# Optimization experiments

Measured on AMD Instinct MI355X. Metric: run time of the kernel, lower is better.

## Reference

```python
import jax, jax.numpy as jnp
import numpy as np

D_MODEL = 1024
D_K = 64
D_V = 64
TEMPERATURE = float(np.sqrt(D_K))
LN_EPS = 1e-5


def setup_inputs() -> dict:
    key = jax.random.key(0)
    ks = jax.random.split(key, 8)
    B, L = 8, 2048
    q = jax.random.normal(ks[0], (B, L, D_K), dtype=jnp.float32)
    k = jax.random.normal(ks[1], (B, L, D_K), dtype=jnp.float32)
    v = jax.random.normal(ks[2], (B, L, D_V), dtype=jnp.float32)
    residual = jax.random.normal(ks[3], (B, L, D_MODEL), dtype=jnp.float32)
    # fc: Linear(d_v, d_model), xavier-normal weight, zero-ish bias
    fc_w = jax.random.normal(ks[4], (D_MODEL, D_V), dtype=jnp.float32) * float(np.sqrt(2.0 / (D_V + D_MODEL)))
    fc_b = jnp.zeros((D_MODEL,), dtype=jnp.float32)
    ln_gamma = jnp.ones((D_MODEL,), dtype=jnp.float32)
    ln_beta = jnp.zeros((D_MODEL,), dtype=jnp.float32)
    return {"q": q, "k": k, "v": v, "residual": residual,
            "fc_w": fc_w, "fc_b": fc_b, "ln_gamma": ln_gamma, "ln_beta": ln_beta}


def reference(q, k, v, residual, fc_w, fc_b, ln_gamma, ln_beta):
    # scaled dot-product attention: scores [B, Lq, Lk]
    scores = jnp.einsum("bqd,bkd->bqk", q, k) / TEMPERATURE
    # module computes both log_softmax and softmax (shared logsumexp in a
    # fused kernel); log_attn is discarded by Attention.forward
    log_attn = jax.nn.log_softmax(scores, axis=2)
    attn = jnp.exp(log_attn)  # == softmax(scores); dropout is identity at eval
    out = jnp.einsum("bqk,bkv->bqv", attn, v)  # [B, Lq, d_v]
    # fc + residual + LayerNorm (dropout identity at eval)
    out = jnp.einsum("bqv,mv->bqm", out, fc_w) + fc_b
    x = out + residual
    mu = jnp.mean(x, axis=-1, keepdims=True)
    var = jnp.var(x, axis=-1, keepdims=True)
    return (x - mu) * jax.lax.rsqrt(var + LN_EPS) * ln_gamma + ln_beta
```

## Files before the change

### kernel.cpp

```cpp
#include <hip/hip_runtime.h>

typedef float  f32x4 __attribute__((ext_vector_type(4)));
typedef float  f4v   __attribute__((ext_vector_type(4)));
typedef short  s16x8 __attribute__((ext_vector_type(8)));
typedef unsigned short u16x4 __attribute__((ext_vector_type(4)));
typedef unsigned short u16x8 __attribute__((ext_vector_type(8)));
typedef unsigned short u16;

#define DEVI static __device__ __forceinline__
#define AS1 __attribute__((address_space(1)))
#define AS3 __attribute__((address_space(3)))

DEVI u16 f2bf(float f) {
  unsigned int u = __builtin_bit_cast(unsigned int, f);
  u += 0x7FFFu + ((u >> 16) & 1u);
  return (u16)(u >> 16);
}

constexpr int B  = 8;
constexpr int L  = 2048;
constexpr int D  = 64;
constexpr int DM = 1024;

__global__ void prep_kernel(const float* __restrict__ k, const float* __restrict__ v,
                            const float* __restrict__ w,
                            u16* __restrict__ kbf, u16* __restrict__ vtbf,
                            u16* __restrict__ wbf) {
  __shared__ float tile[64 * 65];
  const int bid = blockIdx.x, tid = threadIdx.x;
  if (bid < 1024) {
    const int i = bid * 256 + tid;
    f4v f = ((const f4v*)k)[i];
    u16x4 o;
#pragma unroll
    for (int j = 0; j < 4; ++j) o[j] = f2bf(f[j] * 0.18033688f);
    ((u16x4*)kbf)[i] = o;
  } else if (bid < 1024 + 64) {
    const int i = (bid - 1024) * 256 + tid;
    f4v f = ((const f4v*)w)[i];
    u16x4 o;
#pragma unroll
    for (int j = 0; j < 4; ++j) o[j] = f2bf(f[j]);
    ((u16x4*)wbf)[i] = o;
  } else {
    const int t2 = bid - 1088;
    const int b = t2 >> 5, tt = t2 & 31;
    const float* vp = v + ((size_t)b * L + tt * 64) * D;
    for (int i = tid; i < 4096; i += 256) {
      const int r = i >> 6, c = i & 63;
      tile[c * 65 + r] = vp[i];
    }
    __syncthreads();
    u16* op = vtbf + (size_t)b * D * L + tt * 64;
    for (int i = tid; i < 4096; i += 256) {
      const int dv = i >> 6, kv = i & 63;
      op[(size_t)dv * L + kv] = f2bf(tile[dv * 65 + kv]);
    }
  }
}

__global__ __launch_bounds__(512) void attn_kernel(const float* __restrict__ q,
                                                   const u16* __restrict__ kbf,
                                                   const u16* __restrict__ vtbf,
                                                   u16* __restrict__ Og) {
  __shared__ __align__(16) char smem[58 * 1024];
  u16*   Kt   = (u16*)smem;
  u16*   Vt   = (u16*)(smem + 24 * 1024);
  u16*   Pl   = (u16*)(smem + 48 * 1024);
  float* Macc = (float*)smem;
  float* Lsum = (float*)(smem + 35 * 1024);

  const int blk = blockIdx.x;
  const int b = blk & 7;
  const int qrow0 = (blk >> 3) * 64;
  const int tid = threadIdx.x;
  const int wave = tid >> 6, lane = tid & 63;
  const int g = wave >> 1, h = wave & 1;
  const int lg = lane >> 4, ln = lane & 15;

  s16x8 aq[2];
  {
    const float* qp = q + ((size_t)b * L + qrow0 + g * 16 + ln) * D + lg * 8;
#pragma unroll
    for (int kk = 0; kk < 2; ++kk) {
      f4v f0 = *(const f4v*)(qp + kk * 32);
      f4v f1 = *(const f4v*)(qp + kk * 32 + 4);
      s16x8 a;
#pragma unroll
      for (int j = 0; j < 4; ++j) { a[j] = (short)f2bf(f0[j]); a[4 + j] = (short)f2bf(f1[j]); }
      aq[kk] = a;
    }
  }

  const f32x4 zf = {0.f, 0.f, 0.f, 0.f};
  f32x4 acc[4];
#pragma unroll
  for (int i = 0; i < 4; ++i) acc[i] = zf;
  float lrow[4] = {0.f, 0.f, 0.f, 0.f};

  const u16* kb = kbf + (size_t)b * L * D;
  const u16* vb = vtbf + (size_t)b * D * L;

  auto stage = [&](int t) {
    const int buf = t % 3;
    const int kv0 = t * 64;
    const int row = tid >> 3, jl = tid & 7;
    const int js = jl ^ (row & 7);
    const u16* srcK = kb + (size_t)(kv0 + row) * D + js * 8;
    __builtin_amdgcn_global_load_lds(
        (const AS1 unsigned int*)srcK, (AS3 unsigned int*)&Kt[buf * 4096 + tid * 8], 16, 0, 0);
    const u16* srcV = vb + (size_t)row * L + kv0 + js * 8;
    __builtin_amdgcn_global_load_lds(
        (const AS1 unsigned int*)srcV, (AS3 unsigned int*)&Vt[buf * 4096 + tid * 8], 16, 0, 0);
  };

  stage(0);
  stage(1);

  for (int t = 0; t < 32; ++t) {
    if (t < 31) { asm volatile("s_waitcnt vmcnt(2)" ::: "memory"); }
    else        { asm volatile("s_waitcnt vmcnt(0)" ::: "memory"); }
    __builtin_amdgcn_sched_barrier(0);
    __builtin_amdgcn_s_barrier();
    __builtin_amdgcn_sched_barrier(0);
    if (t + 2 < 32) stage(t + 2);
    const int buf = t % 3;

    f32x4 s[2];
    s[0] = zf; s[1] = zf;
#pragma unroll
    for (int kk = 0; kk < 2; ++kk) {
#pragma unroll
      for (int fn2 = 0; fn2 < 2; ++fn2) {
        const int kvr = h * 32 + fn2 * 16 + ln;
        const int j = (kk * 4 + lg) ^ (kvr & 7);
        s16x8 bk = *(const s16x8*)&Kt[buf * 4096 + kvr * 64 + j * 8];
        s[fn2] = __builtin_amdgcn_mfma_f32_16x16x32_bf16(aq[kk], bk, s[fn2], 0, 0, 0);
      }
    }

#pragma unroll
    for (int r = 0; r < 4; ++r) {
      const float p0 = __builtin_amdgcn_exp2f(s[0][r]);
      const float p1 = __builtin_amdgcn_exp2f(s[1][r]);
      lrow[r] += p0 + p1;
      Pl[wave * 640 + (lg * 4 + r) * 40 + ln]      = f2bf(p0);
      Pl[wave * 640 + (lg * 4 + r) * 40 + 16 + ln] = f2bf(p1);
    }

    asm volatile("" ::: "memory");

    s16x8 ap = *(const s16x8*)&Pl[wave * 640 + ln * 40 + lg * 8];
#pragma unroll
    for (int fn = 0; fn < 4; ++fn) {
      const int dv = fn * 16 + ln;
      const int j = (h * 4 + lg) ^ (dv & 7);
      s16x8 bv = *(const s16x8*)&Vt[buf * 4096 + dv * 64 + j * 8];
      acc[fn] = __builtin_amdgcn_mfma_f32_16x16x32_bf16(ap, bv, acc[fn], 0, 0, 0);
    }
  }

  __syncthreads();

#pragma unroll
  for (int r = 0; r < 4; ++r) {
#pragma unroll
    for (int off = 1; off < 16; off <<= 1) lrow[r] += __shfl_xor(lrow[r], off, 64);
    if (ln == 0) Lsum[wave * 16 + lg * 4 + r] = lrow[r];
  }
#pragma unroll
  for (int fn = 0; fn < 4; ++fn)
#pragma unroll
    for (int r = 0; r < 4; ++r)
      Macc[wave * 1088 + (lg * 4 + r) * 68 + fn * 16 + ln] = acc[fn][r];
  __syncthreads();

  {
    const int row = tid >> 3, d0 = (tid & 7) * 8;
    const int g2 = row >> 4, r2 = row & 15;
    const float linv = 1.f / (Lsum[(g2 * 2) * 16 + r2] + Lsum[(g2 * 2 + 1) * 16 + r2]);
    const float* m0p = &Macc[(g2 * 2) * 1088 + r2 * 68 + d0];
    const float* m1p = &Macc[(g2 * 2 + 1) * 1088 + r2 * 68 + d0];
    f4v o0 = *(const f4v*)(m0p)     + *(const f4v*)(m1p);
    f4v o1 = *(const f4v*)(m0p + 4) + *(const f4v*)(m1p + 4);
    u16x8 ob;
#pragma unroll
    for (int j = 0; j < 4; ++j) {
      ob[j]     = f2bf(o0[j] * linv);
      ob[4 + j] = f2bf(o1[j] * linv);
    }
    *(u16x8*)(Og + ((size_t)b * L + qrow0 + row) * D + d0) = ob;
  }
}

__global__ __launch_bounds__(512, 2) void fc_ln_kernel(const u16* __restrict__ Og,
                                                       const u16* __restrict__ wbf,
                                                       const float* __restrict__ bias,
                                                       const float* __restrict__ resid,
                                                       const float* __restrict__ gamma,
                                                       const float* __restrict__ beta,
                                                       float* __restrict__ out) {
  __shared__ __align__(16) u16   Wl[1024 * 64];
  __shared__ __align__(16) float bl[1024];
  __shared__ __align__(16) float gl[1024];
  __shared__ __align__(16) float btl[1024];
  __shared__ float part[8][16][2];

  const int tid = threadIdx.x;
  const int wave = tid >> 6, lane = tid & 63;
  const int rg = wave >> 2, mq = wave & 3;
  const int lg = lane >> 4, ln = lane & 15;
  const int m0 = mq * 256;
  const int vblk = (blockIdx.x & 7) * 32 + (blockIdx.x >> 3);
  const int rowA = vblk * 64 + rg * 16 + ln;
  const int rowB = rowA + 32;
  const int jb = ln & 7;

  {
#pragma unroll
    for (int i = 0; i < 16; ++i) {
      const int c = tid + i * 512;
      const int r = c >> 3, j = c & 7;
      const u16* src = wbf + r * 64 + (j ^ (r & 7)) * 8;
      __builtin_amdgcn_global_load_lds(
          (const AS1 unsigned int*)src, (AS3 unsigned int*)&Wl[c * 8], 16, 0, 0);
    }
    if (tid < 256) {
      __builtin_amdgcn_global_load_lds(
          (const AS1 unsigned int*)(bias + tid * 4), (AS3 unsigned int*)&bl[tid * 4], 16, 0, 0);
      __builtin_amdgcn_global_load_lds(
          (const AS1 unsigned int*)(beta + tid * 4), (AS3 unsigned int*)&btl[tid * 4], 16, 0, 0);
    } else {
      const int t2 = tid - 256;
      __builtin_amdgcn_global_load_lds(
          (const AS1 unsigned int*)(gamma + t2 * 4), (AS3 unsigned int*)&gl[t2 * 4], 16, 0, 0);
    }
  }

  f4v boAr0, boAr1;
  {
    const u16* opA = Og + (size_t)rowA * D + lg * 8;
    asm volatile("global_load_dwordx4 %0, %1, off"           : "=v"(boAr0) : "v"(opA) : "memory");
    asm volatile("global_load_dwordx4 %0, %1, off offset:64" : "=v"(boAr1) : "v"(opA) : "memory");
  }
  f4v rsdA[16];
  {
    const float* rp = resid + (size_t)rowA * DM + m0 + lg * 4;
#pragma unroll
    for (int fn = 0; fn < 16; ++fn)
      asm volatile("global_load_dwordx4 %0, %1, off offset:%c2"
                   : "=v"(rsdA[fn]) : "v"(rp), "i"(fn * 64) : "memory");
  }

  asm volatile("s_waitcnt vmcnt(0)" ::: "memory");
  __builtin_amdgcn_sched_barrier(0);
  __builtin_amdgcn_s_barrier();
  __builtin_amdgcn_sched_barrier(0);

  f32x4 acc[16];
#pragma unroll
  for (int fn = 0; fn < 16; ++fn)
    acc[fn] = *(const f4v*)&bl[m0 + fn * 16 + lg * 4] + rsdA[fn];

  f4v boBr0, boBr1;
  {
    const u16* opB = Og + (size_t)rowB * D + lg * 8;
    asm volatile("global_load_dwordx4 %0, %1, off"           : "=v"(boBr0) : "v"(opB) : "memory");
    asm volatile("global_load_dwordx4 %0, %1, off offset:64" : "=v"(boBr1) : "v"(opB) : "memory");
  }
  f4v rsdB[16];
  {
    const float* rp = resid + (size_t)rowB * DM + m0 + lg * 4;
#pragma unroll
    for (int fn = 0; fn < 16; ++fn)
      asm volatile("global_load_dwordx4 %0, %1, off offset:%c2"
                   : "=v"(rsdB[fn]) : "v"(rp), "i"(fn * 64) : "memory");
  }

  {
    const s16x8 bo0 = __builtin_bit_cast(s16x8, boAr0);
    const s16x8 bo1 = __builtin_bit_cast(s16x8, boAr1);
#pragma unroll
    for (int fn = 0; fn < 16; ++fn) {
      const int m = m0 + fn * 16 + ln;
      s16x8 aw0 = *(const s16x8*)&Wl[m * 64 + (lg ^ jb) * 8];
      s16x8 aw1 = *(const s16x8*)&Wl[m * 64 + ((4 + lg) ^ jb) * 8];
      acc[fn] = __builtin_amdgcn_mfma_f32_16x16x32_bf16(aw0, bo0, acc[fn], 0, 0, 0);
      acc[fn] = __builtin_amdgcn_mfma_f32_16x16x32_bf16(aw1, bo1, acc[fn], 0, 0, 0);
    }
    float sum = 0.f, ssq = 0.f;
#pragma unroll
    for (int fn = 0; fn < 16; ++fn)
#pragma unroll
      for (int r = 0; r < 4; ++r) { const float x = acc[fn][r]; sum += x; ssq += x * x; }
    sum += __shfl_xor(sum, 16, 64); ssq += __shfl_xor(ssq, 16, 64);
    sum += __shfl_xor(sum, 32, 64); ssq += __shfl_xor(ssq, 32, 64);
    if (lg == 0) { part[wave][ln][0] = sum; part[wave][ln][1] = ssq; }
    asm volatile("s_waitcnt lgkmcnt(0)" ::: "memory");
    __builtin_amdgcn_s_barrier();
    __builtin_amdgcn_sched_barrier(0);
    float sm = 0.f, q2 = 0.f;
#pragma unroll
    for (int w2 = 0; w2 < 4; ++w2) { sm += part[rg * 4 + w2][ln][0]; q2 += part[rg * 4 + w2][ln][1]; }
    const float mu   = sm * (1.0f / 1024.0f);
    const float var  = q2 * (1.0f / 1024.0f) - mu * mu;
    const float rstd = rsqrtf(var + 1e-5f);
#pragma unroll
    for (int fn = 0; fn < 16; ++fn) {
      const int m4 = m0 + fn * 16 + lg * 4;
      const f4v gm = *(const f4v*)&gl[m4];
      const f4v bt = *(const f4v*)&btl[m4];
      f4v o;
#pragma unroll
      for (int r = 0; r < 4; ++r) o[r] = (acc[fn][r] - mu) * rstd * gm[r] + bt[r];
      *(f4v*)&out[(size_t)rowA * DM + m4] = o;
    }
  }

  asm volatile("s_waitcnt vmcnt(0)" ::: "memory");
  __builtin_amdgcn_sched_barrier(0);
  __builtin_amdgcn_s_barrier();
  __builtin_amdgcn_sched_barrier(0);

  {
#pragma unroll
    for (int fn = 0; fn < 16; ++fn)
      acc[fn] = *(const f4v*)&bl[m0 + fn * 16 + lg * 4] + rsdB[fn];
    const s16x8 bo0 = __builtin_bit_cast(s16x8, boBr0);
    const s16x8 bo1 = __builtin_bit_cast(s16x8, boBr1);
#pragma unroll
    for (int fn = 0; fn < 16; ++fn) {
      const int m = m0 + fn * 16 + ln;
      s16x8 aw0 = *(const s16x8*)&Wl[m * 64 + (lg ^ jb) * 8];
      s16x8 aw1 = *(const s16x8*)&Wl[m * 64 + ((4 + lg) ^ jb) * 8];
      acc[fn] = __builtin_amdgcn_mfma_f32_16x16x32_bf16(aw0, bo0, acc[fn], 0, 0, 0);
      acc[fn] = __builtin_amdgcn_mfma_f32_16x16x32_bf16(aw1, bo1, acc[fn], 0, 0, 0);
    }
    float sum = 0.f, ssq = 0.f;
#pragma unroll
    for (int fn = 0; fn < 16; ++fn)
#pragma unroll
      for (int r = 0; r < 4; ++r) { const float x = acc[fn][r]; sum += x; ssq += x * x; }
    sum += __shfl_xor(sum, 16, 64); ssq += __shfl_xor(ssq, 16, 64);
    sum += __shfl_xor(sum, 32, 64); ssq += __shfl_xor(ssq, 32, 64);
    if (lg == 0) { part[wave][ln][0] = sum; part[wave][ln][1] = ssq; }
    asm volatile("s_waitcnt lgkmcnt(0)" ::: "memory");
    __builtin_amdgcn_s_barrier();
    __builtin_amdgcn_sched_barrier(0);
    float sm = 0.f, q2 = 0.f;
#pragma unroll
    for (int w2 = 0; w2 < 4; ++w2) { sm += part[rg * 4 + w2][ln][0]; q2 += part[rg * 4 + w2][ln][1]; }
    const float mu   = sm * (1.0f / 1024.0f);
    const float var  = q2 * (1.0f / 1024.0f) - mu * mu;
    const float rstd = rsqrtf(var + 1e-5f);
#pragma unroll
    for (int fn = 0; fn < 16; ++fn) {
      const int m4 = m0 + fn * 16 + lg * 4;
      const f4v gm = *(const f4v*)&gl[m4];
      const f4v bt = *(const f4v*)&btl[m4];
      f4v o;
#pragma unroll
      for (int r = 0; r < 4; ++r) o[r] = (acc[fn][r] - mu) * rstd * gm[r] + bt[r];
      *(f4v*)&out[(size_t)rowB * DM + m4] = o;
    }
  }
}

extern "C" void kernel_launch(void* const* d_in, const int* in_sizes, int n_in,
                              void* d_out, int out_size, void* d_ws, size_t ws_size,
                              hipStream_t stream) {
  const float* q     = (const float*)d_in[0];
  const float* k     = (const float*)d_in[1];
  const float* v     = (const float*)d_in[2];
  const float* resid = (const float*)d_in[3];
  const float* fc_w  = (const float*)d_in[4];
  const float* fc_b  = (const float*)d_in[5];
  const float* gamma = (const float*)d_in[6];
  const float* beta  = (const float*)d_in[7];
  float* out = (float*)d_out;

  char* ws = (char*)d_ws;
  u16*   kbf  = (u16*)(ws);
  u16*   vtbf = (u16*)(ws + (2u << 20));
  u16*   wbf  = (u16*)(ws + (4u << 20));
  u16*   Og   = (u16*)(ws + (4u << 20) + (128u << 10));

  prep_kernel<<<1344, 256, 0, stream>>>(k, v, fc_w, kbf, vtbf, wbf);
  attn_kernel<<<256, 512, 0, stream>>>(q, kbf, vtbf, Og);
  fc_ln_kernel<<<256, 512, 0, stream>>>(Og, wbf, fc_b, resid, gamma, beta, out);
}
```

Before: 58.28 us.

## Drop LDS weight staging in fc_ln; use small 16-row blocks reading weights from cache

```diff
diff --git a/kernel.cpp b/kernel.cpp
--- a/kernel.cpp
+++ b/kernel.cpp
@@ -193,63 +193,47 @@
   }
 }
 
-__global__ __launch_bounds__(512, 2) void fc_ln_kernel(const u16* __restrict__ Og,
+__global__ __launch_bounds__(256, 3) void fc_ln_kernel(const u16* __restrict__ Og,
                                                        const u16* __restrict__ wbf,
                                                        const float* __restrict__ bias,
                                                        const float* __restrict__ resid,
                                                        const float* __restrict__ gamma,
                                                        const float* __restrict__ beta,
                                                        float* __restrict__ out) {
-  __shared__ __align__(16) u16   Wl[1024 * 64];
   __shared__ __align__(16) float bl[1024];
   __shared__ __align__(16) float gl[1024];
   __shared__ __align__(16) float btl[1024];
-  __shared__ float part[8][16][2];
+  __shared__ float part[4][16][2];
 
   const int tid = threadIdx.x;
   const int wave = tid >> 6, lane = tid & 63;
-  const int rg = wave >> 2, mq = wave & 3;
   const int lg = lane >> 4, ln = lane & 15;
-  const int m0 = mq * 256;
-  const int vblk = (blockIdx.x & 7) * 32 + (blockIdx.x >> 3);
-  const int rowA = vblk * 64 + rg * 16 + ln;
-  const int rowB = rowA + 32;
+  const int m0 = wave * 256;
+  const int vblk = (blockIdx.x & 7) * 128 + (blockIdx.x >> 3);
+  const int row = vblk * 16 + ln;
   const int jb = ln & 7;
-
+  (void)jb;
+
+  __builtin_amdgcn_global_load_lds(
+      (const AS1 unsigned int*)(bias + tid * 4), (AS3 unsigned int*)&bl[tid * 4], 16, 0, 0);
+  __builtin_amdgcn_global_load_lds(
+      (const AS1 unsigned int*)(gamma + tid * 4), (AS3 unsigned int*)&gl[tid * 4], 16, 0, 0);
+  __builtin_amdgcn_global_load_lds(
+      (const AS1 unsigned int*)(beta + tid * 4), (AS3 unsigned int*)&btl[tid * 4], 16, 0, 0);
+
+  f4v bo0r, bo1r;
   {
-#pragma unroll
-    for (int i = 0; i < 16; ++i) {
-      const int c = tid + i * 512;
-      const int r = c >> 3, j = c & 7;
-      const u16* src = wbf + r * 64 + (j ^ (r & 7)) * 8;
-      __builtin_amdgcn_global_load_lds(
-          (const AS1 unsigned int*)src, (AS3 unsigned int*)&Wl[c * 8], 16, 0, 0);
-    }
-    if (tid < 256) {
-      __builtin_amdgcn_global_load_lds(
-          (const AS1 unsigned int*)(bias + tid * 4), (AS3 unsigned int*)&bl[tid * 4], 16, 0, 0);
-      __builtin_amdgcn_global_load_lds(
-          (const AS1 unsigned int*)(beta + tid * 4), (AS3 unsigned int*)&btl[tid * 4], 16, 0, 0);
-    } else {
-      const int t2 = tid - 256;
-      __builtin_amdgcn_global_load_lds(
-          (const AS1 unsigned int*)(gamma + t2 * 4), (AS3 unsigned int*)&gl[t2 * 4], 16, 0, 0);
-    }
-  }
-
-  f4v boAr0, boAr1;
+    const u16* op = Og + (size_t)row * D + lg * 8;
+    asm volatile("global_load_dwordx4 %0, %1, off"           : "=v"(bo0r) : "v"(op) : "memory");
+    asm volatile("global_load_dwordx4 %0, %1, off offset:64" : "=v"(bo1r) : "v"(op) : "memory");
+  }
+  f4v rsd[16];
   {
-    const u16* opA = Og + (size_t)rowA * D + lg * 8;
-    asm volatile("global_load_dwordx4 %0, %1, off"           : "=v"(boAr0) : "v"(opA) : "memory");
-    asm volatile("global_load_dwordx4 %0, %1, off offset:64" : "=v"(boAr1) : "v"(opA) : "memory");
-  }
-  f4v rsdA[16];
-  {
-    const float* rp = resid + (size_t)rowA * DM + m0 + lg * 4;
+    const float* rp = resid + (size_t)row * DM + m0 + lg * 4;
 #pragma unroll
     for (int fn = 0; fn < 16; ++fn)
       asm volatile("global_load_dwordx4 %0, %1, off offset:%c2"
-                   : "=v"(rsdA[fn]) : "v"(rp), "i"(fn * 64) : "memory");
+                   : "=v"(rsd[fn]) : "v"(rp), "i"(fn * 64) : "memory");
   }
 
   asm volatile("s_waitcnt vmcnt(0)" ::: "memory");
@@ -257,112 +241,45 @@
   __builtin_amdgcn_s_barrier();
   __builtin_amdgcn_sched_barrier(0);
 
+  const s16x8 bo0 = __builtin_bit_cast(s16x8, bo0r);
+  const s16x8 bo1 = __builtin_bit_cast(s16x8, bo1r);
   f32x4 acc[16];
 #pragma unroll
+  for (int fn = 0; fn < 16; ++fn) {
+    const int m = m0 + fn * 16;
+    const u16* wp = &wbf[(size_t)(m + ln) * D + lg * 8];
+    s16x8 aw0 = *(const s16x8*)(wp);
+    s16x8 aw1 = *(const s16x8*)(wp + 32);
+    acc[fn] = *(const f4v*)&bl[m + lg * 4] + rsd[fn];
+    acc[fn] = __builtin_amdgcn_mfma_f32_16x16x32_bf16(aw0, bo0, acc[fn], 0, 0, 0);
+    acc[fn] = __builtin_amdgcn_mfma_f32_16x16x32_bf16(aw1, bo1, acc[fn], 0, 0, 0);
+  }
+
+  float sum = 0.f, ssq = 0.f;
+#pragma unroll
   for (int fn = 0; fn < 16; ++fn)
-    acc[fn] = *(const f4v*)&bl[m0 + fn * 16 + lg * 4] + rsdA[fn];
-
-  f4v boBr0, boBr1;
-  {
-    const u16* opB = Og + (size_t)rowB * D + lg * 8;
-    asm volatile("global_load_dwordx4 %0, %1, off"           : "=v"(boBr0) : "v"(opB) : "memory");
-    asm volatile("global_load_dwordx4 %0, %1, off offset:64" : "=v"(boBr1) : "v"(opB) : "memory");
-  }
-  f4v rsdB[16];
-  {
-    const float* rp = resid + (size_t)rowB * DM + m0 + lg * 4;
-#pragma unroll
-    for (int fn = 0; fn < 16; ++fn)
-      asm volatile("global_load_dwordx4 %0, %1, off offset:%c2"
-                   : "=v"(rsdB[fn]) : "v"(rp), "i"(fn * 64) : "memory");
-  }
-
-  {
-    const s16x8 bo0 = __builtin_bit_cast(s16x8, boAr0);
-    const s16x8 bo1 = __builtin_bit_cast(s16x8, boAr1);
-#pragma unroll
-    for (int fn = 0; fn < 16; ++fn) {
-      const int m = m0 + fn * 16 + ln;
-      s16x8 aw0 = *(const s16x8*)&Wl[m * 64 + (lg ^ jb) * 8];
-      s16x8 aw1 = *(const s16x8*)&Wl[m * 64 + ((4 + lg) ^ jb) * 8];
-      acc[fn] = __builtin_amdgcn_mfma_f32_16x16x32_bf16(aw0, bo0, acc[fn], 0, 0, 0);
-      acc[fn] = __builtin_amdgcn_mfma_f32_16x16x32_bf16(aw1, bo1, acc[fn], 0, 0, 0);
-    }
-    float sum = 0.f, ssq = 0.f;
-#pragma unroll
-    for (int fn = 0; fn < 16; ++fn)
-#pragma unroll
-      for (int r = 0; r < 4; ++r) { const float x = acc[fn][r]; sum += x; ssq += x * x; }
-    sum += __shfl_xor(sum, 16, 64); ssq += __shfl_xor(ssq, 16, 64);
-    sum += __shfl_xor(sum, 32, 64); ssq += __shfl_xor(ssq, 32, 64);
-    if (lg == 0) { part[wave][ln][0] = sum; part[wave][ln][1] = ssq; }
-    asm volatile("s_waitcnt lgkmcnt(0)" ::: "memory");
-    __builtin_amdgcn_s_barrier();
-    __builtin_amdgcn_sched_barrier(0);
-    float sm = 0.f, q2 = 0.f;
-#pragma unroll
-    for (int w2 = 0; w2 < 4; ++w2) { sm += part[rg * 4 + w2][ln][0]; q2 += part[rg * 4 + w2][ln][1]; }
-    const float mu   = sm * (1.0f / 1024.0f);
-    const float var  = q2 * (1.0f / 1024.0f) - mu * mu;
-    const float rstd = rsqrtf(var + 1e-5f);
-#pragma unroll
-    for (int fn = 0; fn < 16; ++fn) {
-      const int m4 = m0 + fn * 16 + lg * 4;
-      const f4v gm = *(const f4v*)&gl[m4];
-      const f4v bt = *(const f4v*)&btl[m4];
-      f4v o;
-#pragma unroll
-      for (int r = 0; r < 4; ++r) o[r] = (acc[fn][r] - mu) * rstd * gm[r] + bt[r];
-      *(f4v*)&out[(size_t)rowA * DM + m4] = o;
-    }
-  }
-
-  asm volatile("s_waitcnt vmcnt(0)" ::: "memory");
-  __builtin_amdgcn_sched_barrier(0);
-  __builtin_amdgcn_s_barrier();
-  __builtin_amdgcn_sched_barrier(0);
-
-  {
-#pragma unroll
-    for (int fn = 0; fn < 16; ++fn)
-      acc[fn] = *(const f4v*)&bl[m0 + fn * 16 + lg * 4] + rsdB[fn];
-    const s16x8 bo0 = __builtin_bit_cast(s16x8, boBr0);
-    const s16x8 bo1 = __builtin_bit_cast(s16x8, boBr1);
-#pragma unroll
-    for (int fn = 0; fn < 16; ++fn) {
-      const int m = m0 + fn * 16 + ln;
-      s16x8 aw0 = *(const s16x8*)&Wl[m * 64 + (lg ^ jb) * 8];
-      s16x8 aw1 = *(const s16x8*)&Wl[m * 64 + ((4 + lg) ^ jb) * 8];
-      acc[fn] = __builtin_amdgcn_mfma_f32_16x16x32_bf16(aw0, bo0, acc[fn], 0, 0, 0);
-      acc[fn] = __builtin_amdgcn_mfma_f32_16x16x32_bf16(aw1, bo1, acc[fn], 0, 0, 0);
-    }
-    float sum = 0.f, ssq = 0.f;
-#pragma unroll
-    for (int fn = 0; fn < 16; ++fn)
-#pragma unroll
-      for (int r = 0; r < 4; ++r) { const float x = acc[fn][r]; sum += x; ssq += x * x; }
-    sum += __shfl_xor(sum, 16, 64); ssq += __shfl_xor(ssq, 16, 64);
-    sum += __shfl_xor(sum, 32, 64); ssq += __shfl_xor(ssq, 32, 64);
-    if (lg == 0) { part[wave][ln][0] = sum; part[wave][ln][1] = ssq; }
-    asm volatile("s_waitcnt lgkmcnt(0)" ::: "memory");
-    __builtin_amdgcn_s_barrier();
-    __builtin_amdgcn_sched_barrier(0);
-    float sm = 0.f, q2 = 0.f;
-#pragma unroll
-    for (int w2 = 0; w2 < 4; ++w2) { sm += part[rg * 4 + w2][ln][0]; q2 += part[rg * 4 + w2][ln][1]; }
-    const float mu   = sm * (1.0f / 1024.0f);
-    const float var  = q2 * (1.0f / 1024.0f) - mu * mu;
-    const float rstd = rsqrtf(var + 1e-5f);
-#pragma unroll
-    for (int fn = 0; fn < 16; ++fn) {
-      const int m4 = m0 + fn * 16 + lg * 4;
-      const f4v gm = *(const f4v*)&gl[m4];
-      const f4v bt = *(const f4v*)&btl[m4];
-      f4v o;
-#pragma unroll
-      for (int r = 0; r < 4; ++r) o[r] = (acc[fn][r] - mu) * rstd * gm[r] + bt[r];
-      *(f4v*)&out[(size_t)rowB * DM + m4] = o;
-    }
+#pragma unroll
+    for (int r = 0; r < 4; ++r) { const float x = acc[fn][r]; sum += x; ssq += x * x; }
+  sum += __shfl_xor(sum, 16, 64); ssq += __shfl_xor(ssq, 16, 64);
+  sum += __shfl_xor(sum, 32, 64); ssq += __shfl_xor(ssq, 32, 64);
+  if (lg == 0) { part[wave][ln][0] = sum; part[wave][ln][1] = ssq; }
+  __syncthreads();
+  float sm = 0.f, q2 = 0.f;
+#pragma unroll
+  for (int w2 = 0; w2 < 4; ++w2) { sm += part[w2][ln][0]; q2 += part[w2][ln][1]; }
+  const float mu   = sm * (1.0f / 1024.0f);
+  const float var  = q2 * (1.0f / 1024.0f) - mu * mu;
+  const float rstd = rsqrtf(var + 1e-5f);
+
+#pragma unroll
+  for (int fn = 0; fn < 16; ++fn) {
+    const int m4 = m0 + fn * 16 + lg * 4;
+    const f4v gm = *(const f4v*)&gl[m4];
+    const f4v bt = *(const f4v*)&btl[m4];
+    f4v o;
+#pragma unroll
+    for (int r = 0; r < 4; ++r) o[r] = (acc[fn][r] - mu) * rstd * gm[r] + bt[r];
+    *(f4v*)&out[(size_t)row * DM + m4] = o;
   }
 }
 
@@ -387,5 +304,5 @@
 
   prep_kernel<<<1344, 256, 0, stream>>>(k, v, fc_w, kbf, vtbf, wbf);
   attn_kernel<<<256, 512, 0, stream>>>(q, kbf, vtbf, Og);
-  fc_ln_kernel<<<256, 512, 0, stream>>>(Og, wbf, fc_b, resid, gamma, beta, out);
-}
+  fc_ln_kernel<<<(B * L) / 16, 256, 0, stream>>>(Og, wbf, fc_b, resid, gamma, beta, out);
+}
```

Result: slower. 66.84 us (+14.7%).
